# Kernel tuning notes

Measured on AMD Instinct MI355X. Metric: run time of the kernel, lower is better.

The kernel has to match this reference:

```python
import jax, jax.numpy as jnp
import numpy as np

NUM_EMBEDDINGS = 8192
EMBEDDING_DIM = 512
COMMITMENT_COST = 0.1


def setup_inputs() -> dict:
    key = jax.random.key(0)
    k_z, k_cb = jax.random.split(key)
    z = jax.random.normal(k_z, (16, 1024, EMBEDDING_DIM), dtype=jnp.float32)
    # nn.Embedding weight init: uniform(-1/num_embeddings, 1/num_embeddings)
    bound = 1.0 / NUM_EMBEDDINGS
    codebook = jax.random.uniform(
        k_cb, (NUM_EMBEDDINGS, EMBEDDING_DIM), dtype=jnp.float32,
        minval=-bound, maxval=bound)
    return {"z": z, "codebook": codebook}


def reference(z, codebook):
    # z: [B, T, D], codebook: [K, D]
    zf = z.reshape(-1, z.shape[-1])                      # [N, D]
    # squared euclidean distances: ||z||^2 + ||e||^2 - 2 z e^T  -> [N, K]
    distances = (jnp.sum(zf * zf, axis=1, keepdims=True)
                 + jnp.sum(codebook * codebook, axis=1)
                 - 2.0 * jnp.matmul(zf, codebook.T))
    indices = jnp.argmin(distances, axis=1)              # [N]
    z_quantized = codebook[indices].reshape(z.shape)     # [B, T, D]
    zq_sg = jax.lax.stop_gradient(z_quantized)
    commitment_loss = jnp.mean((zq_sg - z) ** 2)
    # mse(z, zq.detach()) == mse(zq.detach(), z) == commitment_loss
    vq_loss = commitment_loss + COMMITMENT_COST * commitment_loss
    # straight-through estimator
    z_st = z + jax.lax.stop_gradient(z_quantized - z)
    return (z_st, vq_loss)
```

## Files before the change

### kernel.cpp

```cpp
#include <hip/hip_runtime.h>


#define M_ROWS 16384
#define K_CODES 8192
#define DIM 512
#define BM 128
#define BN 128
#define BK 128
#define NT (K_CODES / BN)
#define OUT0_SIZE (M_ROWS * DIM)
#define GB_BLOCKS 1024

typedef int   i32x8 __attribute__((ext_vector_type(8)));
typedef float f32x4 __attribute__((ext_vector_type(4)));

template <bool HI>
__device__ __forceinline__ int pk8(float a, float b, int old) {
    return __builtin_amdgcn_cvt_pk_fp8_f32(a, b, old, HI);
}

__global__ __launch_bounds__(256) void convert_all(
    const float* __restrict__ z, const float* __restrict__ cb,
    unsigned char* __restrict__ z8, unsigned char* __restrict__ cb8,
    float* __restrict__ enorm)
{
    const int tid = threadIdx.x;
    if (blockIdx.x < K_CODES / 4) {
        const int w = tid >> 6, lane = tid & 63;
        const int row = blockIdx.x * 4 + w;
        const float* src = cb + (size_t)row * DIM + lane * 8;
        float4 a = *(const float4*)(src);
        float4 b = *(const float4*)(src + 4);
        float ns = a.x * a.x + a.y * a.y + a.z * a.z + a.w * a.w
                 + b.x * b.x + b.y * b.y + b.z * b.z + b.w * b.w;
        const float S = 8192.0f;
        int lo = 0, hi = 0;
        lo = pk8<false>(a.x * S, a.y * S, lo); lo = pk8<true>(a.z * S, a.w * S, lo);
        hi = pk8<false>(b.x * S, b.y * S, hi); hi = pk8<true>(b.z * S, b.w * S, hi);
        *(int2*)(cb8 + (size_t)row * DIM + lane * 8) = make_int2(lo, hi);
        for (int m = 32; m; m >>= 1) ns += __shfl_down(ns, m, 64);
        if (lane == 0) enorm[row] = S * ns;
    } else {
        size_t i = ((size_t)(blockIdx.x - K_CODES / 4) * 256 + tid) * 8;
        float4 a = *(const float4*)(z + i);
        float4 b = *(const float4*)(z + i + 4);
        int lo = 0, hi = 0;
        lo = pk8<false>(a.x, a.y, lo); lo = pk8<true>(a.z, a.w, lo);
        hi = pk8<false>(b.x, b.y, hi); hi = pk8<true>(b.z, b.w, hi);
        *(int2*)(z8 + i) = make_int2(lo, hi);
    }
}

__global__ __launch_bounds__(256, 2) void gemm_argmin(
    const unsigned char* __restrict__ z8, const unsigned char* __restrict__ cb8,
    const float* __restrict__ enorm, unsigned int* __restrict__ candV)
{
    __shared__ alignas(32) unsigned char As[2][BM * BK];
    __shared__ alignas(32) unsigned char Bs[2][BN * BK];
    __shared__ float Es[BN];
    __shared__ unsigned int cU[BM][2];

    const int tid = threadIdx.x;
    const int lane = tid & 63;
    const int w = tid >> 6;
    const int phys = blockIdx.x;
    const int xcd = phys & 7;
    const int idx = phys >> 3;
    const int ktile = idx >> 4;
    const int mtile = xcd * 16 + (idx & 15);
    const int mbase = mtile * BM;
    const int nbase = ktile * BN;

    if (tid < BN) Es[tid] = enorm[nbase + tid];

    f32x4 acc[16];
#pragma unroll
    for (int i = 0; i < 16; ++i) acc[i] = (f32x4){0.f, 0.f, 0.f, 0.f};

    const int rA = lane >> 3;
    const int jG = ((lane & 7) ^ rA) * 16;
    const int quad = lane >> 4;
    const int l15 = lane & 15;
    const int sw = l15 & 7;
    const int rw = (w >> 1) * 64;
    const int cw = (w & 1) * 64;
    const int t32 = ((quad << 1) ^ (sw & 6)) * 16;

#define STAGE(buf, dt_) do {                                                  \
    _Pragma("unroll")                                                         \
    for (int i_ = 0; i_ < 4; ++i_) {                                          \
        int c_ = w * 4 + i_;                                                  \
        int row_ = c_ * 8 + rA;                                               \
        const unsigned char* ga_ = z8 + (size_t)(mbase + row_) * DIM + (dt_) * BK + jG; \
        const unsigned char* gb_ = cb8 + (size_t)(nbase + row_) * DIM + (dt_) * BK + jG; \
        unsigned char* la_ = As[buf] + c_ * 1024 + lane * 16;                 \
        unsigned char* lb_ = Bs[buf] + c_ * 1024 + lane * 16;                 \
        __builtin_amdgcn_global_load_lds((const __attribute__((address_space(1))) void*)ga_, \
                                         (__attribute__((address_space(3))) void*)la_, 16, 0, 0); \
        __builtin_amdgcn_global_load_lds((const __attribute__((address_space(1))) void*)gb_, \
                                         (__attribute__((address_space(3))) void*)lb_, 16, 0, 0); \
    } } while (0)

    STAGE(0, 0);
    __syncthreads();

#pragma unroll
    for (int dt = 0; dt < 4; ++dt) {
        const int cur = dt & 1;
        if (dt < 3) STAGE(cur ^ 1, dt + 1);
        i32x8 bfr[4];
#pragma unroll
        for (int cf = 0; cf < 4; ++cf)
            bfr[cf] = *(const i32x8*)(Bs[cur] + (cw + cf * 16 + l15) * BK + t32);
#pragma unroll
        for (int rf = 0; rf < 4; ++rf) {
            i32x8 a = *(const i32x8*)(As[cur] + (rw + rf * 16 + l15) * BK + t32);
#pragma unroll
            for (int cf = 0; cf < 4; ++cf)
                acc[rf * 4 + cf] = __builtin_amdgcn_mfma_scale_f32_16x16x128_f8f6f4(
                    a, bfr[cf], acc[rf * 4 + cf],
                    0, 0,
                    0, 0x7F7F7F7F,
                    0, 0x7F7F7F7F);
        }
        __syncthreads();
    }
#undef STAGE

    float es[4];
#pragma unroll
    for (int cf = 0; cf < 4; ++cf) es[cf] = Es[cw + cf * 16 + l15];

#pragma unroll
    for (int rf = 0; rf < 4; ++rf) {
#pragma unroll
        for (int r = 0; r < 4; ++r) {
            float bv = 3.4e38f; int bi = 0;
#pragma unroll
            for (int cf = 0; cf < 4; ++cf) {
                int col = cw + cf * 16 + l15;
                float dist = fmaf(-2.0f, acc[rf * 4 + cf][r], es[cf]);
                if (dist < bv) { bv = dist; bi = col; }
            }
            unsigned u = __builtin_bit_cast(unsigned, bv);
            u ^= ((unsigned)(((int)u) >> 31)) | 0x80000000u;
            unsigned key = (u & 0xFFFFE000u) | (unsigned)(nbase + bi);
#pragma unroll
            for (int m = 1; m < 16; m <<= 1) {
                unsigned o = __shfl_xor(key, m, 64);
                key = o < key ? o : key;
            }
            if (l15 == 0) cU[rw + rf * 16 + quad * 4 + r][w & 1] = key;
        }
    }
    __syncthreads();
    if (tid < BM) {
        unsigned k0 = cU[tid][0], k1 = cU[tid][1];
        candV[(size_t)ktile * M_ROWS + mbase + tid] = k0 < k1 ? k0 : k1;
    }
}

__global__ __launch_bounds__(256) void gather_out(
    const float* __restrict__ z, const float* __restrict__ cb,
    const unsigned int* __restrict__ candV, float* __restrict__ out,
    float* __restrict__ partials)
{
    __shared__ float red[4];
    const int tid = threadIdx.x;
    const int w = tid >> 6, lane = tid & 63;
    float lsum = 0.f;
#pragma unroll
    for (int it = 0; it < M_ROWS / (GB_BLOCKS * 4); ++it) {
        int row = (it * GB_BLOCKS + blockIdx.x) * 4 + w;
        unsigned key = candV[(size_t)lane * M_ROWS + row];
#pragma unroll
        for (int m = 1; m < 64; m <<= 1) {
            unsigned o = __shfl_xor(key, m, 64);
            key = o < key ? o : key;
        }
        int k = (int)(key & 8191u);
#pragma unroll
        for (int j = 0; j < 2; ++j) {
            int slot = lane + j * 64;
            float4 zv = ((const float4*)(z + (size_t)row * DIM))[slot];
            float4 cv = ((const float4*)(cb + (size_t)k * DIM))[slot];
            float dx = cv.x - zv.x, dy = cv.y - zv.y;
            float dz2 = cv.z - zv.z, dw = cv.w - zv.w;
            float4 o = {zv.x + dx, zv.y + dy, zv.z + dz2, zv.w + dw};
            ((float4*)(out + (size_t)row * DIM))[slot] = o;
            lsum += dx * dx + dy * dy + dz2 * dz2 + dw * dw;
        }
    }
    for (int m = 32; m; m >>= 1) lsum += __shfl_down(lsum, m, 64);
    if (lane == 0) red[w] = lsum;
    __syncthreads();
    if (tid == 0) partials[blockIdx.x] = (red[0] + red[1]) + (red[2] + red[3]);
}

__global__ __launch_bounds__(256) void reduce_loss(
    const float* __restrict__ partials, float* __restrict__ lossOut)
{
    __shared__ float red[4];
    const int tid = threadIdx.x;
    float s = 0.f;
#pragma unroll
    for (int i = 0; i < GB_BLOCKS / 256; ++i) s += partials[i * 256 + tid];
    for (int m = 32; m; m >>= 1) s += __shfl_down(s, m, 64);
    if ((tid & 63) == 0) red[tid >> 6] = s;
    __syncthreads();
    if (tid == 0)
        lossOut[0] = ((red[0] + red[1]) + (red[2] + red[3])) * (1.1f / (float)OUT0_SIZE);
}

extern "C" void kernel_launch(void* const* d_in, const int* in_sizes, int n_in,
                              void* d_out, int out_size, void* d_ws, size_t ws_size,
                              hipStream_t stream) {
    const float* z = (const float*)d_in[0];
    const float* cb = (const float*)d_in[1];
    float* out = (float*)d_out;
    char* ws = (char*)d_ws;

    unsigned char* z8   = (unsigned char*)(ws);
    unsigned char* cb8  = (unsigned char*)(ws + 8388608);
    float* enorm        = (float*)(ws + 12582912);
    unsigned int* candV = (unsigned int*)(ws + 12615680);
    float* partials     = (float*)(ws + 16809984);

    convert_all<<<K_CODES / 4 + M_ROWS * DIM / 2048, 256, 0, stream>>>(
        z, cb, z8, cb8, enorm);
    gemm_argmin<<<NT * (M_ROWS / BM), 256, 0, stream>>>(z8, cb8, enorm, candV);
    gather_out<<<GB_BLOCKS, 256, 0, stream>>>(z, cb, candV, out, partials);
    reduce_loss<<<1, 256, 0, stream>>>(partials, out + OUT0_SIZE);
}
```

Baseline: 255.2 us.

## Keep codebook tile resident in LDS and loop over eight row tiles

The GEMM-argmin kernel now loads the full 128x512 codebook tile into LDS once per block, then streams eight consecutive z row tiles through a double-buffered A buffer. Blocks grow to 512 threads (8 waves, 64x32 per wave), the grid shrinks by a factor of eight, and the enorm values are read straight into registers. This aims to cut repeated codebook loads and per-block launch and epilogue overhead. In exchange, LDS use is larger, occupancy drops to one block per CU, there are fewer blocks to spread across the GPU, and synchronisation relies on hand-placed barriers and vmcnt waits.

```diff
diff --git a/kernel.cpp b/kernel.cpp
--- a/kernel.cpp
+++ b/kernel.cpp
@@ -7,6 +7,8 @@
 #define BM 128
 #define BN 128
 #define BK 128
+#define KSTEPS 4
+#define G_MT 8
 #define NT (K_CODES / BN)
 #define OUT0_SIZE (M_ROWS * DIM)
 #define GB_BLOCKS 1024
@@ -17,6 +19,11 @@
 template <bool HI>
 __device__ __forceinline__ int pk8(float a, float b, int old) {
     return __builtin_amdgcn_cvt_pk_fp8_f32(a, b, old, HI);
+}
+
+__device__ __forceinline__ void gload_lds(const unsigned char* g, unsigned char* l) {
+    __builtin_amdgcn_global_load_lds((const __attribute__((address_space(1))) void*)g,
+                                     (__attribute__((address_space(3))) void*)l, 16, 0, 0);
 }
 
 __global__ __launch_bounds__(256) void convert_all(
@@ -51,113 +58,118 @@
     }
 }
 
-__global__ __launch_bounds__(256, 2) void gemm_argmin(
+__global__ __launch_bounds__(512, 1) void gemm_argmin(
     const unsigned char* __restrict__ z8, const unsigned char* __restrict__ cb8,
     const float* __restrict__ enorm, unsigned int* __restrict__ candV)
 {
+    __shared__ alignas(32) unsigned char Bs[KSTEPS][BN * BK];
     __shared__ alignas(32) unsigned char As[2][BM * BK];
-    __shared__ alignas(32) unsigned char Bs[2][BN * BK];
-    __shared__ float Es[BN];
-    __shared__ unsigned int cU[BM][2];
+    __shared__ unsigned int cU[BM][4];
 
     const int tid = threadIdx.x;
     const int lane = tid & 63;
     const int w = tid >> 6;
-    const int phys = blockIdx.x;
-    const int xcd = phys & 7;
-    const int idx = phys >> 3;
-    const int ktile = idx >> 4;
-    const int mtile = xcd * 16 + (idx & 15);
-    const int mbase = mtile * BM;
+    const int b = blockIdx.x;
+    const int xcd = b & 7;
+    const int idx = b >> 3;
+    const int ktile = xcd * 8 + (idx >> 4);
+    const int mgroup = idx & 15;
     const int nbase = ktile * BN;
-
-    if (tid < BN) Es[tid] = enorm[nbase + tid];
-
-    f32x4 acc[16];
-#pragma unroll
-    for (int i = 0; i < 16; ++i) acc[i] = (f32x4){0.f, 0.f, 0.f, 0.f};
 
     const int rA = lane >> 3;
     const int jG = ((lane & 7) ^ rA) * 16;
     const int quad = lane >> 4;
     const int l15 = lane & 15;
     const int sw = l15 & 7;
-    const int rw = (w >> 1) * 64;
-    const int cw = (w & 1) * 64;
+    const int wr = (w >> 2) * 64;
+    const int wc = (w & 3) * 32;
     const int t32 = ((quad << 1) ^ (sw & 6)) * 16;
 
-#define STAGE(buf, dt_) do {                                                  \
+    float es0 = enorm[nbase + wc + l15];
+    float es1 = enorm[nbase + wc + 16 + l15];
+
+#pragma unroll
+    for (int ks = 0; ks < KSTEPS; ++ks)
+#pragma unroll
+        for (int i = 0; i < 2; ++i) {
+            int c = w * 2 + i;
+            int row = c * 8 + rA;
+            gload_lds(cb8 + (size_t)(nbase + row) * DIM + ks * BK + jG,
+                      Bs[ks] + c * 1024 + lane * 16);
+        }
+
+#define STAGE_A(slot, m_, k_) do {                                            \
     _Pragma("unroll")                                                         \
-    for (int i_ = 0; i_ < 4; ++i_) {                                          \
-        int c_ = w * 4 + i_;                                                  \
+    for (int i_ = 0; i_ < 2; ++i_) {                                          \
+        int c_ = w * 2 + i_;                                                  \
         int row_ = c_ * 8 + rA;                                               \
-        const unsigned char* ga_ = z8 + (size_t)(mbase + row_) * DIM + (dt_) * BK + jG; \
-        const unsigned char* gb_ = cb8 + (size_t)(nbase + row_) * DIM + (dt_) * BK + jG; \
-        unsigned char* la_ = As[buf] + c_ * 1024 + lane * 16;                 \
-        unsigned char* lb_ = Bs[buf] + c_ * 1024 + lane * 16;                 \
-        __builtin_amdgcn_global_load_lds((const __attribute__((address_space(1))) void*)ga_, \
-                                         (__attribute__((address_space(3))) void*)la_, 16, 0, 0); \
-        __builtin_amdgcn_global_load_lds((const __attribute__((address_space(1))) void*)gb_, \
-                                         (__attribute__((address_space(3))) void*)lb_, 16, 0, 0); \
+        gload_lds(z8 + (size_t)((mgroup * G_MT + (m_)) * BM + row_) * DIM     \
+                     + (k_) * BK + jG,                                        \
+                  As[slot] + c_ * 1024 + lane * 16);                          \
     } } while (0)
 
-    STAGE(0, 0);
-    __syncthreads();
-
-#pragma unroll
-    for (int dt = 0; dt < 4; ++dt) {
-        const int cur = dt & 1;
-        if (dt < 3) STAGE(cur ^ 1, dt + 1);
-        i32x8 bfr[4];
-#pragma unroll
-        for (int cf = 0; cf < 4; ++cf)
-            bfr[cf] = *(const i32x8*)(Bs[cur] + (cw + cf * 16 + l15) * BK + t32);
+    STAGE_A(0, 0, 0);
+
+    for (int m = 0; m < G_MT; ++m) {
+        f32x4 acc[8];
+#pragma unroll
+        for (int i = 0; i < 8; ++i) acc[i] = (f32x4){0.f, 0.f, 0.f, 0.f};
+
+#pragma unroll
+        for (int k = 0; k < KSTEPS; ++k) {
+            __builtin_amdgcn_s_barrier();
+            __builtin_amdgcn_sched_barrier(0);
+            if (k < KSTEPS - 1) {
+                STAGE_A((k + 1) & 1, m, k + 1);
+                asm volatile("s_waitcnt vmcnt(2)" ::: "memory");
+            } else if (m < G_MT - 1) {
+                STAGE_A(0, m + 1, 0);
+                asm volatile("s_waitcnt vmcnt(2)" ::: "memory");
+            } else {
+                asm volatile("s_waitcnt vmcnt(0)" ::: "memory");
+            }
+            i32x8 bf0 = *(const i32x8*)(Bs[k] + (wc + l15) * BK + t32);
+            i32x8 bf1 = *(const i32x8*)(Bs[k] + (wc + 16 + l15) * BK + t32);
+#pragma unroll
+            for (int rf = 0; rf < 4; ++rf) {
+                i32x8 a = *(const i32x8*)(As[k & 1] + (wr + rf * 16 + l15) * BK + t32);
+                acc[rf * 2 + 0] = __builtin_amdgcn_mfma_scale_f32_16x16x128_f8f6f4(
+                    a, bf0, acc[rf * 2 + 0], 0, 0, 0, 0x7F7F7F7F, 0, 0x7F7F7F7F);
+                acc[rf * 2 + 1] = __builtin_amdgcn_mfma_scale_f32_16x16x128_f8f6f4(
+                    a, bf1, acc[rf * 2 + 1], 0, 0, 0, 0x7F7F7F7F, 0, 0x7F7F7F7F);
+            }
+        }
+
+        const int mb = (mgroup * G_MT + m) * BM;
 #pragma unroll
         for (int rf = 0; rf < 4; ++rf) {
-            i32x8 a = *(const i32x8*)(As[cur] + (rw + rf * 16 + l15) * BK + t32);
-#pragma unroll
-            for (int cf = 0; cf < 4; ++cf)
-                acc[rf * 4 + cf] = __builtin_amdgcn_mfma_scale_f32_16x16x128_f8f6f4(
-                    a, bfr[cf], acc[rf * 4 + cf],
-                    0, 0,
-                    0, 0x7F7F7F7F,
-                    0, 0x7F7F7F7F);
+#pragma unroll
+            for (int r = 0; r < 4; ++r) {
+                float d0 = fmaf(-2.0f, acc[rf * 2 + 0][r], es0);
+                float d1 = fmaf(-2.0f, acc[rf * 2 + 1][r], es1);
+                float bv = d1 < d0 ? d1 : d0;
+                int col = d1 < d0 ? wc + 16 + l15 : wc + l15;
+                unsigned u = __builtin_bit_cast(unsigned, bv);
+                u ^= ((unsigned)(((int)u) >> 31)) | 0x80000000u;
+                unsigned key = (u & 0xFFFFE000u) | (unsigned)(nbase + col);
+#pragma unroll
+                for (int sh = 1; sh < 16; sh <<= 1) {
+                    unsigned o = __shfl_xor(key, sh, 64);
+                    key = o < key ? o : key;
+                }
+                if (l15 == 0) cU[wr + rf * 16 + quad * 4 + r][w & 3] = key;
+            }
         }
         __syncthreads();
+        if (tid < BM) {
+            unsigned k0 = cU[tid][0], k1 = cU[tid][1];
+            unsigned k2 = cU[tid][2], k3 = cU[tid][3];
+            unsigned ka = k0 < k1 ? k0 : k1;
+            unsigned kb = k2 < k3 ? k2 : k3;
+            candV[(size_t)ktile * M_ROWS + mb + tid] = ka < kb ? ka : kb;
+        }
     }
-#undef STAGE
-
-    float es[4];
-#pragma unroll
-    for (int cf = 0; cf < 4; ++cf) es[cf] = Es[cw + cf * 16 + l15];
-
-#pragma unroll
-    for (int rf = 0; rf < 4; ++rf) {
-#pragma unroll
-        for (int r = 0; r < 4; ++r) {
-            float bv = 3.4e38f; int bi = 0;
-#pragma unroll
-            for (int cf = 0; cf < 4; ++cf) {
-                int col = cw + cf * 16 + l15;
-                float dist = fmaf(-2.0f, acc[rf * 4 + cf][r], es[cf]);
-                if (dist < bv) { bv = dist; bi = col; }
-            }
-            unsigned u = __builtin_bit_cast(unsigned, bv);
-            u ^= ((unsigned)(((int)u) >> 31)) | 0x80000000u;
-            unsigned key = (u & 0xFFFFE000u) | (unsigned)(nbase + bi);
-#pragma unroll
-            for (int m = 1; m < 16; m <<= 1) {
-                unsigned o = __shfl_xor(key, m, 64);
-                key = o < key ? o : key;
-            }
-            if (l15 == 0) cU[rw + rf * 16 + quad * 4 + r][w & 1] = key;
-        }
-    }
-    __syncthreads();
-    if (tid < BM) {
-        unsigned k0 = cU[tid][0], k1 = cU[tid][1];
-        candV[(size_t)ktile * M_ROWS + mbase + tid] = k0 < k1 ? k0 : k1;
-    }
+#undef STAGE_A
 }
 
 __global__ __launch_bounds__(256) void gather_out(
@@ -228,7 +240,7 @@
 
     convert_all<<<K_CODES / 4 + M_ROWS * DIM / 2048, 256, 0, stream>>>(
         z, cb, z8, cb8, enorm);
-    gemm_argmin<<<NT * (M_ROWS / BM), 256, 0, stream>>>(z8, cb8, enorm, candV);
+    gemm_argmin<<<NT * (M_ROWS / BM) / G_MT, 512, 0, stream>>>(z8, cb8, enorm, candV);
     gather_out<<<GB_BLOCKS, 256, 0, stream>>>(z, cb, candV, out, partials);
     reduce_loss<<<1, 256, 0, stream>>>(partials, out + OUT0_SIZE);
 }
```

Result: slower. 315.7 us (+23.7%).
